# Kernel tuning notes

Hardware: AMD Instinct MI355X
Metric: run time of the kernel (lower is better)

The kernel has to match this reference:

```python
import jax, jax.numpy as jnp
import numpy as np
from math import factorial

RS1 = [(16, 0), (8, 1), (4, 2)]
RS2 = [(16, 0), (8, 1), (4, 2)]


def _su2_cg(j1, j2, j3, m1, m2, m3):
    # Clebsch-Gordan coefficient <j1 m1 j2 m2 | j3 m3> (integer j's)
    if m3 != m1 + m2:
        return 0.0
    f = factorial
    vmin = int(max(-j1 + j2 + m3, -j1 + m1, 0))
    vmax = int(min(j2 + j3 + m1, j3 - j1 + j2, j3 + m3))
    C = ((2.0 * j3 + 1.0) * f(j3 + j1 - j2) * f(j3 - j1 + j2) * f(j1 + j2 - j3)
         * f(j3 + m3) * f(j3 - m3)
         / (f(j1 + j2 + j3 + 1) * f(j1 - m1) * f(j1 + m1) * f(j2 - m2) * f(j2 + m2))) ** 0.5
    S = 0.0
    for v in range(vmin, vmax + 1):
        S += (-1.0) ** (v + j2 + m2) * f(j2 + j3 + m1 - v) * f(j1 - m1 + v) \
             / (f(v) * f(j3 - j1 + j2 - v) * f(j3 + m3 - v) * f(v + j1 - j2 - m3))
    return C * S


def _su2_tensor(j1, j2, j3):
    C = np.zeros((2 * j1 + 1, 2 * j2 + 1, 2 * j3 + 1))
    for m1 in range(-j1, j1 + 1):
        for m2 in range(-j2, j2 + 1):
            m3 = m1 + m2
            if abs(m3) <= j3:
                C[m1 + j1, m2 + j2, m3 + j3] = _su2_cg(j1, j2, j3, m1, m2, m3)
    return C


def _change_basis_real_to_complex(l):
    q = np.zeros((2 * l + 1, 2 * l + 1), dtype=np.complex128)
    for m in range(-l, 0):
        q[l + m, l + abs(m)] = 2 ** -0.5
        q[l + m, l - abs(m)] = -1j * 2 ** -0.5
    q[l, l] = 1.0
    for m in range(1, l + 1):
        q[l + m, l + abs(m)] = (-1) ** m * 2 ** -0.5
        q[l + m, l - abs(m)] = 1j * (-1) ** m * 2 ** -0.5
    return ((-1j) ** l) * q


def _real_cg(l1, l2, l3):
    # CG tensor in the real spherical-harmonic basis, shape (2l1+1, 2l2+1, 2l3+1)
    C = _su2_tensor(l1, l2, l3)
    Q1 = _change_basis_real_to_complex(l1)
    Q2 = _change_basis_real_to_complex(l2)
    Q3 = _change_basis_real_to_complex(l3)
    C = np.einsum('ij,kl,mn,ikn->jlm', Q1, Q2, np.conj(Q3.T), C)
    return np.real(C)


def build_mixing_matrix(Rs1, Rs2):
    dim_in1 = sum(mul * (2 * l + 1) for mul, l in Rs1)
    dim_in2 = sum(mul * (2 * l + 1) for mul, l in Rs2)
    K = sum(m1 * m2 * (2 * l + 1)
            for m1, l1 in Rs1 for m2, l2 in Rs2
            for l in range(abs(l1 - l2), l1 + l2 + 1))
    M = np.zeros((K, dim_in1, dim_in2), dtype=np.float32)
    k_off = 0
    i_off = 0
    for mul1, l1 in Rs1:
        d1 = 2 * l1 + 1
        j_off = 0
        for mul2, l2 in Rs2:
            d2 = 2 * l2 + 1
            for l in range(abs(l1 - l2), l1 + l2 + 1):
                dl = 2 * l + 1
                # 'component' normalization
                C = (_real_cg(l1, l2, l) * (dl ** 0.5)).astype(np.float32)
                Ck = np.transpose(C, (2, 0, 1))  # (dl, d1, d2)
                for u in range(mul1):
                    for v in range(mul2):
                        k0 = k_off + (u * mul2 + v) * dl
                        M[k0:k0 + dl,
                          i_off + u * d1:i_off + (u + 1) * d1,
                          j_off + v * d2:j_off + (v + 1) * d2] = Ck
                k_off += mul1 * mul2 * dl
            j_off += mul2 * d2
        i_off += mul1 * d1
    return M


def setup_inputs() -> dict:
    key = jax.random.key(0)
    k1, k2 = jax.random.split(key)
    Z = 4096
    f1 = jax.random.normal(k1, (Z, 60), dtype=jnp.float32)
    f2 = jax.random.normal(k2, (Z, 60), dtype=jnp.float32)
    mix = jnp.asarray(build_mixing_matrix(RS1, RS2))  # (3600, 60, 60)
    return {"features_1": f1, "features_2": f2, "mixing_matrix": mix}


def reference(features_1, features_2, mixing_matrix):
    # output[z, k] = sum_{i,j} C[k,i,j] * f1[z,i] * f2[z,j]
    Z = features_1.shape[0]
    K, I, J = mixing_matrix.shape
    outer = jnp.einsum('zi,zj->zij', features_1, features_2).reshape(Z, I * J)
    return outer @ mixing_matrix.reshape(K, I * J).T
```

## Files before the change

kernel.cpp:

```cpp
#include <hip/hip_runtime.h>


#define ZT    64
#define ZPAD  68
#define NF    60
#define KTOT  3600
#define BLOCK 256
#define NLD   ((ZT * NF) / 4)

typedef float f32x4 __attribute__((ext_vector_type(4)));

struct Seg { short kstart, mul2, dl, d1, d2, ioff, joff, pad; };

__constant__ Seg c_segs[19] = {
  {   0,16,1,1,1, 0, 0,0},
  { 256, 8,3,1,3, 0,16,0},
  { 640, 4,5,1,5, 0,40,0},
  { 960,16,3,3,1,16, 0,0},
  {1344, 8,1,3,3,16,16,0},
  {1408, 8,3,3,3,16,16,0},
  {1600, 8,5,3,3,16,16,0},
  {1920, 4,3,3,5,16,40,0},
  {2016, 4,5,3,5,16,40,0},
  {2176, 4,7,3,5,16,40,0},
  {2400,16,5,5,1,40, 0,0},
  {2720, 8,3,5,3,40,16,0},
  {2816, 8,5,5,3,40,16,0},
  {2976, 8,7,5,3,40,16,0},
  {3200, 4,1,5,5,40,40,0},
  {3216, 4,3,5,5,40,40,0},
  {3264, 4,5,5,5,40,40,0},
  {3344, 4,7,5,5,40,40,0},
  {3456, 4,9,5,5,40,40,0}
};

__constant__ short c_kwmap[15][4] = {
  {50,30, 4, 0}, {51,31, 5, 1}, {52,32, 6, 2}, {53,33, 7, 3},
  {54,34,10,-1}, {55,35,11,-1}, {56,36,12,-1},
  {37,43, 8,15}, {44,45, 9,16}, {46,47,17,18}, {48,49,19,20},
  {13,14,21,22}, {23,24,25,26}, {27,28,29,38}, {39,40,41,42}
};

template<int D1, int D2>
__device__ __forceinline__ void load_c(float (&c)[25],
    const float* __restrict__ Crow, int i0, int j0)
{
#pragma unroll
  for (int ii = 0; ii < D1; ++ii)
#pragma unroll
    for (int jj = 0; jj < D2; ++jj)
      c[ii * D2 + jj] = Crow[(i0 + ii) * NF + (j0 + jj)];
}

template<int D1, int D2>
__device__ __forceinline__ void ld_ab(f32x4 (&a)[D1], f32x4 (&b)[D2],
    const float (&f1s)[NF][ZPAD], const float (&f2s)[NF][ZPAD],
    int i0, int j0, int zz)
{
#pragma unroll
  for (int ii = 0; ii < D1; ++ii) a[ii] = *(const f32x4*)&f1s[i0 + ii][zz];
#pragma unroll
  for (int jj = 0; jj < D2; ++jj) b[jj] = *(const f32x4*)&f2s[j0 + jj][zz];
}

template<int D1, int D2>
__device__ __forceinline__ void comp_st(const float (&c)[25],
    const f32x4 (&a)[D1], const f32x4 (&b)[D2], float* __restrict__ opz)
{
#pragma unroll
  for (int q = 0; q < 4; ++q) {
    float acc;
    if constexpr (D1 <= D2) {
      acc = 0.f;
#pragma unroll
      for (int ii = 0; ii < D1; ++ii) {
        float t = c[ii * D2] * b[0][q];
#pragma unroll
        for (int jj = 1; jj < D2; ++jj) t = fmaf(c[ii * D2 + jj], b[jj][q], t);
        acc = fmaf(t, a[ii][q], acc);
      }
    } else {
      acc = 0.f;
#pragma unroll
      for (int jj = 0; jj < D2; ++jj) {
        float t = c[jj] * a[0][q];
#pragma unroll
        for (int ii = 1; ii < D1; ++ii) t = fmaf(c[ii * D2 + jj], a[ii][q], t);
        acc = fmaf(t, b[jj][q], acc);
      }
    }
    __builtin_nontemporal_store(acc, opz + (size_t)q * KTOT);
  }
}

template<int D1, int D2>
__device__ void tp_body(const float (&c)[25], int i0, int j0,
    const float (&f1s)[NF][ZPAD], const float (&f2s)[NF][ZPAD],
    float* __restrict__ op)
{
  f32x4 aA[D1], bA[D2], aB[D1], bB[D2];
  ld_ab<D1,D2>(aA, bA, f1s, f2s, i0, j0, 0);
#pragma unroll 1
  for (int zz = 0; zz < ZT; zz += 8) {
    ld_ab<D1,D2>(aB, bB, f1s, f2s, i0, j0, zz + 4);
    comp_st<D1,D2>(c, aA, bA, op + (size_t)zz * KTOT);
    if (zz + 8 < ZT) ld_ab<D1,D2>(aA, bA, f1s, f2s, i0, j0, zz + 8);
    comp_st<D1,D2>(c, aB, bB, op + (size_t)(zz + 4) * KTOT);
  }
}

__global__ __launch_bounds__(BLOCK, 3) void tp_kernel(
    const float* __restrict__ f1, const float* __restrict__ f2,
    const float* __restrict__ M, float* __restrict__ out)
{
  __shared__ __align__(16) float f1s[NF][ZPAD];
  __shared__ __align__(16) float f2s[NF][ZPAD];
  const int z0  = blockIdx.y * ZT;
  const int tid = (int)threadIdx.x;

  const float* f1p = f1 + (size_t)z0 * NF;
  const float* f2p = f2 + (size_t)z0 * NF;
  f32x4 s1[4], s2[4];
#pragma unroll
  for (int r = 0; r < 4; ++r) {
    int t = tid + r * BLOCK;
    if (t < NLD) {
      s1[r] = *(const f32x4*)(f1p + t * 4);
      s2[r] = *(const f32x4*)(f2p + t * 4);
    }
  }

  const int wv   = tid >> 6;
  const int lane = tid & 63;
  const int kw   = (int)c_kwmap[blockIdx.x][wv];
  const int k    = (kw << 6) + lane;
  const bool active = (kw >= 0) && (k < KTOT);
  const int kc = active ? k : 0;
  int s = 0;
  s += (kc >=  256); s += (kc >=  640); s += (kc >=  960); s += (kc >= 1344);
  s += (kc >= 1408); s += (kc >= 1600); s += (kc >= 1920); s += (kc >= 2016);
  s += (kc >= 2176); s += (kc >= 2400); s += (kc >= 2720); s += (kc >= 2816);
  s += (kc >= 2976); s += (kc >= 3200); s += (kc >= 3216); s += (kc >= 3264);
  s += (kc >= 3344); s += (kc >= 3456);
  const Seg sg = c_segs[s];
  const int local = kc - sg.kstart;
  const int uv = local / sg.dl;
  const int u  = uv / sg.mul2;
  const int v  = uv - u * sg.mul2;
  const int i0 = sg.ioff + u * sg.d1;
  const int j0 = sg.joff + v * sg.d2;
  const float* Crow = M + (size_t)kc * (NF * NF);

  float c[25];
  const int d1 = sg.d1, d2 = sg.d2;
  if (d1 == 1) {
    if (d2 == 1)      load_c<1,1>(c, Crow, i0, j0);
    else if (d2 == 3) load_c<1,3>(c, Crow, i0, j0);
    else              load_c<1,5>(c, Crow, i0, j0);
  } else if (d1 == 3) {
    if (d2 == 1)      load_c<3,1>(c, Crow, i0, j0);
    else if (d2 == 3) load_c<3,3>(c, Crow, i0, j0);
    else              load_c<3,5>(c, Crow, i0, j0);
  } else {
    if (d2 == 1)      load_c<5,1>(c, Crow, i0, j0);
    else if (d2 == 3) load_c<5,3>(c, Crow, i0, j0);
    else              load_c<5,5>(c, Crow, i0, j0);
  }

#pragma unroll
  for (int r = 0; r < 4; ++r) {
    int t = tid + r * BLOCK;
    if (t < NLD) {
      int g = t * 4, zz = g / NF, f0 = g % NF;
      f1s[f0 + 0][zz] = s1[r][0]; f1s[f0 + 1][zz] = s1[r][1];
      f1s[f0 + 2][zz] = s1[r][2]; f1s[f0 + 3][zz] = s1[r][3];
      f2s[f0 + 0][zz] = s2[r][0]; f2s[f0 + 1][zz] = s2[r][1];
      f2s[f0 + 2][zz] = s2[r][2]; f2s[f0 + 3][zz] = s2[r][3];
    }
  }
  __syncthreads();

  if (!active) return;
  float* op = out + (size_t)z0 * KTOT + k;

  if (d1 == 1) {
    if (d2 == 1)      tp_body<1,1>(c, i0, j0, f1s, f2s, op);
    else if (d2 == 3) tp_body<1,3>(c, i0, j0, f1s, f2s, op);
    else              tp_body<1,5>(c, i0, j0, f1s, f2s, op);
  } else if (d1 == 3) {
    if (d2 == 1)      tp_body<3,1>(c, i0, j0, f1s, f2s, op);
    else if (d2 == 3) tp_body<3,3>(c, i0, j0, f1s, f2s, op);
    else              tp_body<3,5>(c, i0, j0, f1s, f2s, op);
  } else {
    if (d2 == 1)      tp_body<5,1>(c, i0, j0, f1s, f2s, op);
    else if (d2 == 3) tp_body<5,3>(c, i0, j0, f1s, f2s, op);
    else              tp_body<5,5>(c, i0, j0, f1s, f2s, op);
  }
}

extern "C" void kernel_launch(void* const* d_in, const int* in_sizes, int n_in,
                              void* d_out, int out_size, void* d_ws, size_t ws_size,
                              hipStream_t stream) {
  const float* f1 = (const float*)d_in[0];
  const float* f2 = (const float*)d_in[1];
  const float* M  = (const float*)d_in[2];
  float* out = (float*)d_out;

  const int Z = in_sizes[0] / NF;
  dim3 grid(15, Z / ZT);
  tp_kernel<<<grid, dim3(BLOCK), 0, stream>>>(f1, f2, M, out);
}
```

Before: 24.60 us.

## Halve z-tile, raise occupancy, rotate wave-to-k mapping, use normal stores

Shrinks the per-block z tile from 64 to 32 rows, which doubles the grid and halves the LDS footprint, and raises the launch-bounds occupancy hint from 3 to 4 blocks. Rotates which k-wave each warp handles by blockIdx.y so that the idle wave slots and the uneven per-wave work are spread across SIMDs. Replaces nontemporal output stores with ordinary stores. The cost is twice as many blocks, each repeating the mixing-matrix coefficient loads and the k decode, and it tightens the register budget.

```diff
diff --git a/kernel.cpp b/kernel.cpp
--- a/kernel.cpp
+++ b/kernel.cpp
@@ -1,8 +1,8 @@
 #include <hip/hip_runtime.h>
 
 
-#define ZT    64
-#define ZPAD  68
+#define ZT    32
+#define ZPAD  36
 #define NF    60
 #define KTOT  3600
 #define BLOCK 256
@@ -13,24 +13,12 @@
 struct Seg { short kstart, mul2, dl, d1, d2, ioff, joff, pad; };
 
 __constant__ Seg c_segs[19] = {
-  {   0,16,1,1,1, 0, 0,0},
-  { 256, 8,3,1,3, 0,16,0},
-  { 640, 4,5,1,5, 0,40,0},
-  { 960,16,3,3,1,16, 0,0},
-  {1344, 8,1,3,3,16,16,0},
-  {1408, 8,3,3,3,16,16,0},
-  {1600, 8,5,3,3,16,16,0},
-  {1920, 4,3,3,5,16,40,0},
-  {2016, 4,5,3,5,16,40,0},
-  {2176, 4,7,3,5,16,40,0},
-  {2400,16,5,5,1,40, 0,0},
-  {2720, 8,3,5,3,40,16,0},
-  {2816, 8,5,5,3,40,16,0},
-  {2976, 8,7,5,3,40,16,0},
-  {3200, 4,1,5,5,40,40,0},
-  {3216, 4,3,5,5,40,40,0},
-  {3264, 4,5,5,5,40,40,0},
-  {3344, 4,7,5,5,40,40,0},
+  {   0,16,1,1,1, 0, 0,0}, { 256, 8,3,1,3, 0,16,0}, { 640, 4,5,1,5, 0,40,0},
+  { 960,16,3,3,1,16, 0,0}, {1344, 8,1,3,3,16,16,0}, {1408, 8,3,3,3,16,16,0},
+  {1600, 8,5,3,3,16,16,0}, {1920, 4,3,3,5,16,40,0}, {2016, 4,5,3,5,16,40,0},
+  {2176, 4,7,3,5,16,40,0}, {2400,16,5,5,1,40, 0,0}, {2720, 8,3,5,3,40,16,0},
+  {2816, 8,5,5,3,40,16,0}, {2976, 8,7,5,3,40,16,0}, {3200, 4,1,5,5,40,40,0},
+  {3216, 4,3,5,5,40,40,0}, {3264, 4,5,5,5,40,40,0}, {3344, 4,7,5,5,40,40,0},
   {3456, 4,9,5,5,40,40,0}
 };
 
@@ -41,6 +29,22 @@
   {13,14,21,22}, {23,24,25,26}, {27,28,29,38}, {39,40,41,42}
 };
 
+__device__ __forceinline__ void decode_k(int kc, Seg& sg, int& i0, int& j0) {
+  int s = 0;
+  s += (kc >=  256); s += (kc >=  640); s += (kc >=  960); s += (kc >= 1344);
+  s += (kc >= 1408); s += (kc >= 1600); s += (kc >= 1920); s += (kc >= 2016);
+  s += (kc >= 2176); s += (kc >= 2400); s += (kc >= 2720); s += (kc >= 2816);
+  s += (kc >= 2976); s += (kc >= 3200); s += (kc >= 3216); s += (kc >= 3264);
+  s += (kc >= 3344); s += (kc >= 3456);
+  sg = c_segs[s];
+  const int local = kc - sg.kstart;
+  const int uv = local / sg.dl;
+  const int u  = uv / sg.mul2;
+  const int v  = uv - u * sg.mul2;
+  i0 = sg.ioff + u * sg.d1;
+  j0 = sg.joff + v * sg.d2;
+}
+
 template<int D1, int D2>
 __device__ __forceinline__ void load_c(float (&c)[25],
     const float* __restrict__ Crow, int i0, int j0)
@@ -89,7 +93,7 @@
         acc = fmaf(t, b[jj][q], acc);
       }
     }
-    __builtin_nontemporal_store(acc, opz + (size_t)q * KTOT);
+    opz[(size_t)q * KTOT] = acc;
   }
 }
 
@@ -109,7 +113,7 @@
   }
 }
 
-__global__ __launch_bounds__(BLOCK, 3) void tp_kernel(
+__global__ __launch_bounds__(BLOCK, 4) void tp_kernel(
     const float* __restrict__ f1, const float* __restrict__ f2,
     const float* __restrict__ M, float* __restrict__ out)
 {
@@ -120,35 +124,24 @@
 
   const float* f1p = f1 + (size_t)z0 * NF;
   const float* f2p = f2 + (size_t)z0 * NF;
-  f32x4 s1[4], s2[4];
-#pragma unroll
-  for (int r = 0; r < 4; ++r) {
-    int t = tid + r * BLOCK;
+  f32x4 s1[2], s2[2];
+#pragma unroll
+  for (int r = 0; r < 2; ++r) {
+    const int t = tid + r * BLOCK;
     if (t < NLD) {
-      s1[r] = *(const f32x4*)(f1p + t * 4);
-      s2[r] = *(const f32x4*)(f2p + t * 4);
+      s1[r] = *(const f32x4*)(f1p + 4 * t);
+      s2[r] = *(const f32x4*)(f2p + 4 * t);
     }
   }
 
   const int wv   = tid >> 6;
   const int lane = tid & 63;
-  const int kw   = (int)c_kwmap[blockIdx.x][wv];
+  const int kw   = (int)c_kwmap[blockIdx.x][(wv + (int)blockIdx.y) & 3];
   const int k    = (kw << 6) + lane;
   const bool active = (kw >= 0) && (k < KTOT);
   const int kc = active ? k : 0;
-  int s = 0;
-  s += (kc >=  256); s += (kc >=  640); s += (kc >=  960); s += (kc >= 1344);
-  s += (kc >= 1408); s += (kc >= 1600); s += (kc >= 1920); s += (kc >= 2016);
-  s += (kc >= 2176); s += (kc >= 2400); s += (kc >= 2720); s += (kc >= 2816);
-  s += (kc >= 2976); s += (kc >= 3200); s += (kc >= 3216); s += (kc >= 3264);
-  s += (kc >= 3344); s += (kc >= 3456);
-  const Seg sg = c_segs[s];
-  const int local = kc - sg.kstart;
-  const int uv = local / sg.dl;
-  const int u  = uv / sg.mul2;
-  const int v  = uv - u * sg.mul2;
-  const int i0 = sg.ioff + u * sg.d1;
-  const int j0 = sg.joff + v * sg.d2;
+  Seg sg; int i0, j0;
+  decode_k(kc, sg, i0, j0);
   const float* Crow = M + (size_t)kc * (NF * NF);
 
   float c[25];
@@ -168,19 +161,19 @@
   }
 
 #pragma unroll
-  for (int r = 0; r < 4; ++r) {
-    int t = tid + r * BLOCK;
+  for (int r = 0; r < 2; ++r) {
+    const int t = tid + r * BLOCK;
     if (t < NLD) {
-      int g = t * 4, zz = g / NF, f0 = g % NF;
-      f1s[f0 + 0][zz] = s1[r][0]; f1s[f0 + 1][zz] = s1[r][1];
-      f1s[f0 + 2][zz] = s1[r][2]; f1s[f0 + 3][zz] = s1[r][3];
-      f2s[f0 + 0][zz] = s2[r][0]; f2s[f0 + 1][zz] = s2[r][1];
-      f2s[f0 + 2][zz] = s2[r][2]; f2s[f0 + 3][zz] = s2[r][3];
+      const int g = 4 * t, zz = g / NF, f0 = g % NF;
+      f1s[f0+0][zz] = s1[r][0]; f1s[f0+1][zz] = s1[r][1];
+      f1s[f0+2][zz] = s1[r][2]; f1s[f0+3][zz] = s1[r][3];
+      f2s[f0+0][zz] = s2[r][0]; f2s[f0+1][zz] = s2[r][1];
+      f2s[f0+2][zz] = s2[r][2]; f2s[f0+3][zz] = s2[r][3];
     }
   }
   __syncthreads();
-
   if (!active) return;
+
   float* op = out + (size_t)z0 * KTOT + k;
 
   if (d1 == 1) {
```

Measured after the change: 27.35 us. 11.2% more time.
